# Optimization experiments

Hardware: AMD Instinct MI355X
Metric: run time of the kernel (lower is better)

Reference implementation:

```python
import jax, jax.numpy as jnp
import numpy as np

B, C, H, W = 4, 256, 64, 64
C8 = C // 8

def setup_inputs() -> dict:
    key = jax.random.key(0)
    ks = jax.random.split(key, 7)
    s = 0.05
    return {
        "x": jax.random.normal(ks[0], (B, C, H, W), dtype=jnp.float32),
        "wq": jax.random.normal(ks[1], (C8, C), dtype=jnp.float32) * s,
        "bq": jax.random.normal(ks[2], (C8,), dtype=jnp.float32) * s,
        "wk": jax.random.normal(ks[3], (C8, C), dtype=jnp.float32) * s,
        "bk": jax.random.normal(ks[4], (C8,), dtype=jnp.float32) * s,
        "wv": jax.random.normal(ks[5], (C, C), dtype=jnp.float32) * s,
        "bv": jax.random.normal(ks[6], (C,), dtype=jnp.float32) * s,
    }

def reference(x, wq, bq, wk, bk, wv, bv):
    b, c, h, w = x.shape
    n = h * w
    xf = x.reshape(b, c, n)                                   # [B,C,N]
    q = jnp.einsum('oc,bcn->bon', wq, xf) + bq[:, None]       # [B,C/8,N]
    k = jnp.einsum('oc,bcn->bon', wk, xf) + bk[:, None]       # [B,C/8,N]
    v = jnp.einsum('oc,bcn->bon', wv, xf) + bv[:, None]       # [B,C,N]
    # attention[b, i, j] = softmax_j( q[b,:,i] . k[b,:,j] )  (no scaling, per original)
    scores = jnp.einsum('bon,bom->bnm', q, k)                 # [B,N,N]
    attn = jax.nn.softmax(scores, axis=-1)
    # out[b,c,i] = sum_j v[b,c,j] * attn[b,i,j]
    out = jnp.einsum('bcm,bnm->bcn', v, attn)                 # [B,C,N]
    return out.reshape(b, c, h, w) + x
```

## Files before the change

### kernel.cpp

```cpp
#include <hip/hip_runtime.h>
#include <cstdint>
#include <cstddef>

#define BB 4
#define CC 256
#define NN 4096
#define CO 32

typedef __attribute__((ext_vector_type(8))) short bf8;
typedef __attribute__((ext_vector_type(4))) float f4;
typedef __attribute__((ext_vector_type(16))) float f16f;
typedef __attribute__((ext_vector_type(2))) unsigned int u32x2;

#define AS1 __attribute__((address_space(1)))
#define AS3 __attribute__((address_space(3)))

__device__ __forceinline__ unsigned short f2bf(float f) {
    union { float f; unsigned int u; } c; c.f = f;
    unsigned int r = c.u + 0x7FFFu + ((c.u >> 16) & 1u);
    return (unsigned short)(r >> 16);
}
__device__ __forceinline__ float bf2f(unsigned short b) {
    union { unsigned int u; float f; } c; c.u = ((unsigned int)b) << 16;
    return c.f;
}
__device__ __forceinline__ unsigned int cvt_pk_bf16(float a, float b) {
    unsigned int r;
    asm("v_cvt_pk_bf16_f32 %0, %1, %2" : "=v"(r) : "v"(a), "v"(b));
    return r;
}

__global__ __launch_bounds__(512, 2) void k_prep(
        const float* __restrict__ x,
        const float* __restrict__ wq, const float* __restrict__ bq,
        const float* __restrict__ wk, const float* __restrict__ bk,
        const float* __restrict__ wv, const float* __restrict__ bv,
        unsigned short* __restrict__ q_hi, unsigned short* __restrict__ q_lo,
        unsigned short* __restrict__ k_hi, unsigned short* __restrict__ k_lo,
        unsigned short* __restrict__ vws) {
    __shared__ float xT[64 * 256];
    int blk = blockIdx.x;
    int it = blk & 63, b = blk >> 6;
    int i0 = it * 64;
    int tid = threadIdx.x, w = tid >> 6, lane = tid & 63;
    int lr = lane & 15, lg = lane >> 4;

    {
        const float* xp = x + (size_t)b * CC * NN + i0;
        int cl = tid >> 4;
        int il = (tid & 15) * 4;
#pragma unroll
        for (int pass = 0; pass < 8; ++pass) {
            int c = pass * 32 + cl;
            f4 v = *(const f4*)(xp + (size_t)c * NN + il);
#pragma unroll
            for (int jj = 0; jj < 4; ++jj) {
                int i = il + jj;
                xT[i * 256 + (((c >> 2) ^ (i & 7)) << 2) + (c & 3)] = v[jj];
            }
        }
    }
    __syncthreads();

    if (w < 4) {
        f4 acc[4] = {};
        for (int ks = 0; ks < 8; ++ks) {
            int i = w * 16 + lr;
            int kc = ks * 32 + lg * 8;
            f4 xa = *(const f4*)&xT[i * 256 + (((kc >> 2) ^ (i & 7)) << 2)];
            f4 xb = *(const f4*)&xT[i * 256 + ((((kc >> 2) + 1) ^ (i & 7)) << 2)];
            bf8 ahi, alo;
#pragma unroll
            for (int e = 0; e < 8; ++e) {
                float f = (e < 4) ? xa[e] : xb[e - 4];
                unsigned short hh = f2bf(f);
                ahi[e] = (short)hh;
                alo[e] = (short)f2bf(f - bf2f(hh));
            }
#pragma unroll
            for (int u = 0; u < 4; ++u) {
                int o = u * 16 + lr;
                const float* wrow = (u < 2) ? (wq + (size_t)o * CC)
                                            : (wk + (size_t)(o - 32) * CC);
                bf8 bhi, blo;
#pragma unroll
                for (int e = 0; e < 8; ++e) {
                    float wvv = wrow[ks * 32 + lg * 8 + e];
                    unsigned short hh = f2bf(wvv);
                    bhi[e] = (short)hh;
                    blo[e] = (short)f2bf(wvv - bf2f(hh));
                }
                acc[u] = __builtin_amdgcn_mfma_f32_16x16x32_bf16(alo, bhi, acc[u], 0, 0, 0);
                acc[u] = __builtin_amdgcn_mfma_f32_16x16x32_bf16(ahi, blo, acc[u], 0, 0, 0);
                acc[u] = __builtin_amdgcn_mfma_f32_16x16x32_bf16(ahi, bhi, acc[u], 0, 0, 0);
            }
        }
#pragma unroll
        for (int u = 0; u < 4; ++u) {
            int o = u * 16 + lr;
            float bias = (u < 2) ? bq[o] : bk[o - 32];
#pragma unroll
            for (int r = 0; r < 4; ++r) {
                int i = i0 + w * 16 + lg * 4 + r;
                float v = acc[u][r] + bias;
                unsigned short hh = f2bf(v);
                unsigned short ll = f2bf(v - bf2f(hh));
                if (u < 2) {
                    size_t off = ((size_t)b * NN + i) * CO + o;
                    q_hi[off] = hh; q_lo[off] = ll;
                } else {
                    size_t off = ((size_t)b * NN + i) * CO + (o - 32);
                    k_hi[off] = hh; k_lo[off] = ll;
                }
            }
        }
    } else {
        int cb = (w - 4) * 64;
        f4 acc[4][4];
#pragma unroll
        for (int u = 0; u < 4; ++u) {
            f4 bias4;
#pragma unroll
            for (int r = 0; r < 4; ++r) bias4[r] = bv[cb + u * 16 + lg * 4 + r];
#pragma unroll
            for (int t = 0; t < 4; ++t) acc[u][t] = bias4;
        }
        for (int ks = 0; ks < 8; ++ks) {
            bf8 bfr[4];
#pragma unroll
            for (int t = 0; t < 4; ++t) {
                int i = t * 16 + lr;
                int kc = ks * 32 + lg * 8;
                f4 xa = *(const f4*)&xT[i * 256 + (((kc >> 2) ^ (i & 7)) << 2)];
                f4 xb = *(const f4*)&xT[i * 256 + ((((kc >> 2) + 1) ^ (i & 7)) << 2)];
#pragma unroll
                for (int e = 0; e < 8; ++e)
                    bfr[t][e] = (short)f2bf((e < 4) ? xa[e] : xb[e - 4]);
            }
#pragma unroll
            for (int u = 0; u < 4; ++u) {
                const float* wrow = wv + (size_t)(cb + u * 16 + lr) * CC + ks * 32 + lg * 8;
                bf8 afr;
#pragma unroll
                for (int e = 0; e < 8; ++e) afr[e] = (short)f2bf(wrow[e]);
#pragma unroll
                for (int t = 0; t < 4; ++t)
                    acc[u][t] = __builtin_amdgcn_mfma_f32_16x16x32_bf16(afr, bfr[t], acc[u][t], 0, 0, 0);
            }
        }
#pragma unroll
        for (int u = 0; u < 4; ++u)
#pragma unroll
            for (int t = 0; t < 4; ++t)
#pragma unroll
                for (int r = 0; r < 4; ++r) {
                    int c = cb + u * 16 + lg * 4 + r;
                    vws[((size_t)b * CC + c) * NN + i0 + t * 16 + lr] = f2bf(acc[u][t][r]);
                }
    }
}

__global__ __launch_bounds__(512, 4) void k_attn(
        const unsigned short* __restrict__ q_hi, const unsigned short* __restrict__ q_lo,
        const unsigned short* __restrict__ k_hi, const unsigned short* __restrict__ k_lo,
        const unsigned short* __restrict__ vws,
        const float* __restrict__ x, float* __restrict__ out) {
    __shared__ __align__(16) unsigned short Vt[2][16384];
    __shared__ __align__(16) unsigned short K2[4096];
    __shared__ __align__(16) unsigned short Pt[2048];
    __shared__ float lsum_s[4][32];

    int m = blockIdx.x;
    int xcd = m & 7;
    int b = xcd >> 1;
    int qblk = ((m >> 3) << 1) + (xcd & 1);
    int i0 = qblk * 32;
    int tid = threadIdx.x, w = tid >> 6, lane = tid & 63;
    int lr = lane & 15, lg = lane >> 4, lr7 = lr & 7;
    int qh = w & 1, jq = w >> 1;
    int l31 = lane & 31, hh = lane >> 5;

    bf8 qfh, qfl;
    {
        size_t off = ((size_t)b * NN + i0 + qh * 16 + lr) * CO + lg * 8;
        qfh = *(const bf8*)(q_hi + off);
        qfl = *(const bf8*)(q_lo + off);
    }

    int l3 = lane >> 3, sl = lane & 7;
    int us = sl ^ l3;
    const unsigned short* kbase = (us < 4) ? (k_hi + (size_t)b * NN * CO + us * 8)
                                           : (k_lo + (size_t)b * NN * CO + (us - 4) * 8);
    const unsigned short* ksrc = kbase + (size_t)(w * 8 + l3) * CO;
    const unsigned short* vsrc = vws + ((size_t)b * CC + w * 32 + l3) * NN + us * 8;

    auto stageK = [&](int jt) {
        int j0 = ((jt < 64) ? jt : 63) * 64;
        __builtin_amdgcn_global_load_lds((const AS1 void*)(ksrc + (size_t)j0 * CO),
            (AS3 void*)(&K2[(w * 8) * 64]), 16, 0, 0);
    };
    auto stageV = [&](int jt, int p) {
        int j0 = ((jt < 64) ? jt : 63) * 64;
#pragma unroll
        for (int n = 0; n < 4; ++n) {
            __builtin_amdgcn_global_load_lds((const AS1 void*)(vsrc + (size_t)(n * 8) * NN + j0),
                (AS3 void*)(&Vt[p][(w * 32 + n * 8) * 64]), 16, 0, 0);
        }
    };

    f16f acc = {};
    float lsum = 0.f;

    stageK(0);
    stageV(0, 0);
    __syncthreads();

    int prow_swz = (l31 ^ (l31 >> 3)) & 7;
    int vrow_swz = l31 & 7;

    for (int jt = 0; jt < 64; ++jt) {
        int pv = jt & 1;
        {
            int jl = jq * 16 + lr;
            const unsigned short* Kp = &K2[jl * 64];
            bf8 kfh = *(const bf8*)(Kp + ((lg ^ lr7)) * 8);
            bf8 kfl = *(const bf8*)(Kp + (((4 | lg) ^ lr7)) * 8);
            f4 s = {};
            s = __builtin_amdgcn_mfma_f32_16x16x32_bf16(kfh, qfl, s, 0, 0, 0);
            s = __builtin_amdgcn_mfma_f32_16x16x32_bf16(kfl, qfh, s, 0, 0, 0);
            s = __builtin_amdgcn_mfma_f32_16x16x32_bf16(kfh, qfh, s, 0, 0, 0);
            float e0 = __expf(s[0]), e1 = __expf(s[1]), e2 = __expf(s[2]), e3 = __expf(s[3]);
            lsum += (e0 + e1) + (e2 + e3);
            u32x2 d;
            d[0] = cvt_pk_bf16(e0, e1);
            d[1] = cvt_pk_bf16(e2, e3);
            int row = qh * 16 + lr;
            int swz = (row ^ (row >> 3)) & 7;
            int slot = (jq * 2 + (lg >> 1)) ^ swz;
            *(u32x2*)&Pt[row * 64 + slot * 8 + (lg & 1) * 4] = d;
        }
        __builtin_amdgcn_sched_barrier(0);
        asm volatile("s_waitcnt vmcnt(0) lgkmcnt(0)" ::: "memory");
        __builtin_amdgcn_s_barrier();
        __builtin_amdgcn_sched_barrier(0);
        stageK(jt + 1);
        __builtin_amdgcn_s_setprio(1);
        {
            const unsigned short* Pr = &Pt[l31 * 64];
            const unsigned short* Vr = &Vt[pv][(w * 32 + l31) * 64];
#pragma unroll
            for (int kc = 0; kc < 4; ++kc) {
                bf8 pb = *(const bf8*)(Pr + (((kc * 2 + hh) ^ prow_swz)) * 8);
                bf8 vf = *(const bf8*)(Vr + (((kc * 2 + hh) ^ vrow_swz)) * 8);
                acc = __builtin_amdgcn_mfma_f32_32x32x16_bf16(vf, pb, acc, 0, 0, 0);
            }
        }
        __builtin_amdgcn_s_setprio(0);
        stageV(jt + 1, pv ^ 1);
        __builtin_amdgcn_sched_barrier(0);
        asm volatile("s_waitcnt vmcnt(4) lgkmcnt(0)" ::: "memory");
        __builtin_amdgcn_s_barrier();
        __builtin_amdgcn_sched_barrier(0);
    }

    lsum += __shfl_xor(lsum, 16, 64);
    lsum += __shfl_xor(lsum, 32, 64);
    if (lane < 16) lsum_s[jq][qh * 16 + lane] = lsum;
    __syncthreads();

    float linv = 1.0f / (((lsum_s[0][l31] + lsum_s[1][l31]) +
                          (lsum_s[2][l31] + lsum_s[3][l31])));
    int iq = i0 + l31;
#pragma unroll
    for (int r = 0; r < 16; ++r) {
        int c = w * 32 + (r & 3) + 8 * (r >> 2) + 4 * hh;
        size_t off = ((size_t)(b * CC + c)) * NN + iq;
        out[off] = acc[r] * linv + x[off];
    }
}

extern "C" void kernel_launch(void* const* d_in, const int* in_sizes, int n_in,
                              void* d_out, int out_size, void* d_ws, size_t ws_size,
                              hipStream_t stream) {
    const float* x  = (const float*)d_in[0];
    const float* wq = (const float*)d_in[1];
    const float* bq = (const float*)d_in[2];
    const float* wk = (const float*)d_in[3];
    const float* bk = (const float*)d_in[4];
    const float* wv = (const float*)d_in[5];
    const float* bv = (const float*)d_in[6];
    float* out = (float*)d_out;
    char* ws = (char*)d_ws;
    unsigned short* qh = (unsigned short*)(ws);
    unsigned short* ql = (unsigned short*)(ws + 1048576);
    unsigned short* kh = (unsigned short*)(ws + 2097152);
    unsigned short* kl = (unsigned short*)(ws + 3145728);
    unsigned short* vv = (unsigned short*)(ws + 4194304);

    hipLaunchKernelGGL(k_prep, dim3(256), dim3(512), 0, stream,
                       x, wq, bq, wk, bk, wv, bv, qh, ql, kh, kl, vv);
    hipLaunchKernelGGL(k_attn, dim3(512), dim3(512), 0, stream,
                       qh, ql, kh, kl, vv, x, out);
}
```

Before: 103.5 us.

## Double query tile per block and software-pipeline QK softmax ahead of PV

After: 110.1 us. +6.4%, slower.

```diff
diff --git a/kernel.cpp b/kernel.cpp
--- a/kernel.cpp
+++ b/kernel.cpp
@@ -160,29 +160,30 @@
     }
 }
 
-__global__ __launch_bounds__(512, 4) void k_attn(
+__global__ __launch_bounds__(512, 1) void k_attn(
         const unsigned short* __restrict__ q_hi, const unsigned short* __restrict__ q_lo,
         const unsigned short* __restrict__ k_hi, const unsigned short* __restrict__ k_lo,
         const unsigned short* __restrict__ vws,
         const float* __restrict__ x, float* __restrict__ out) {
     __shared__ __align__(16) unsigned short Vt[2][16384];
-    __shared__ __align__(16) unsigned short K2[4096];
-    __shared__ __align__(16) unsigned short Pt[2048];
-    __shared__ float lsum_s[4][32];
+    __shared__ __align__(16) unsigned short K2[2][4096];
+    __shared__ __align__(16) unsigned short Pt[2][4096];
+    __shared__ float lsum_s[2][64];
 
     int m = blockIdx.x;
     int xcd = m & 7;
     int b = xcd >> 1;
     int qblk = ((m >> 3) << 1) + (xcd & 1);
-    int i0 = qblk * 32;
+    int i0 = qblk * 64;
     int tid = threadIdx.x, w = tid >> 6, lane = tid & 63;
     int lr = lane & 15, lg = lane >> 4, lr7 = lr & 7;
-    int qh = w & 1, jq = w >> 1;
+    int a = w & 3, h = w >> 2;
     int l31 = lane & 31, hh = lane >> 5;
+    int cw = w & 3, qg = w >> 2;
 
     bf8 qfh, qfl;
     {
-        size_t off = ((size_t)b * NN + i0 + qh * 16 + lr) * CO + lg * 8;
+        size_t off = ((size_t)b * NN + i0 + a * 16 + lr) * CO + lg * 8;
         qfh = *(const bf8*)(q_hi + off);
         qfl = *(const bf8*)(q_lo + off);
     }
@@ -194,10 +195,10 @@
     const unsigned short* ksrc = kbase + (size_t)(w * 8 + l3) * CO;
     const unsigned short* vsrc = vws + ((size_t)b * CC + w * 32 + l3) * NN + us * 8;
 
-    auto stageK = [&](int jt) {
+    auto stageK = [&](int jt, int p) {
         int j0 = ((jt < 64) ? jt : 63) * 64;
         __builtin_amdgcn_global_load_lds((const AS1 void*)(ksrc + (size_t)j0 * CO),
-            (AS3 void*)(&K2[(w * 8) * 64]), 16, 0, 0);
+            (AS3 void*)(&K2[p][(w * 8) * 64]), 16, 0, 0);
     };
     auto stageV = [&](int jt, int p) {
         int j0 = ((jt < 64) ? jt : 63) * 64;
@@ -208,21 +209,15 @@
         }
     };
 
-    f16f acc = {};
+    f16f acc0 = {}, acc1 = {};
     float lsum = 0.f;
 
-    stageK(0);
-    stageV(0, 0);
-    __syncthreads();
-
-    int prow_swz = (l31 ^ (l31 >> 3)) & 7;
-    int vrow_swz = l31 & 7;
-
-    for (int jt = 0; jt < 64; ++jt) {
-        int pv = jt & 1;
-        {
-            int jl = jq * 16 + lr;
-            const unsigned short* Kp = &K2[jl * 64];
+    auto S_phase = [&](int js) {
+        int pk = js & 1;
+#pragma unroll
+        for (int t = 0; t < 2; ++t) {
+            int jl = h * 32 + t * 16 + lr;
+            const unsigned short* Kp = &K2[pk][jl * 64];
             bf8 kfh = *(const bf8*)(Kp + ((lg ^ lr7)) * 8);
             bf8 kfl = *(const bf8*)(Kp + (((4 | lg) ^ lr7)) * 8);
             f4 s = {};
@@ -234,48 +229,67 @@
             u32x2 d;
             d[0] = cvt_pk_bf16(e0, e1);
             d[1] = cvt_pk_bf16(e2, e3);
-            int row = qh * 16 + lr;
+            int row = a * 16 + lr;
             int swz = (row ^ (row >> 3)) & 7;
-            int slot = (jq * 2 + (lg >> 1)) ^ swz;
-            *(u32x2*)&Pt[row * 64 + slot * 8 + (lg & 1) * 4] = d;
-        }
+            int slot = (h * 4 + t * 2 + (lg >> 1)) ^ swz;
+            *(u32x2*)&Pt[pk][row * 64 + slot * 8 + (lg & 1) * 4] = d;
+        }
+    };
+    auto PV_phase = [&](int jt) {
+        int pv = jt & 1;
+        int prow = qg * 32 + l31;
+        int pswz = (prow ^ (prow >> 3)) & 7;
+        const unsigned short* Pr  = &Pt[pv][prow * 64];
+        const unsigned short* Vr0 = &Vt[pv][(cw * 64 + l31) * 64];
+        const unsigned short* Vr1 = &Vt[pv][(cw * 64 + 32 + l31) * 64];
+        int vswz = l31 & 7;
+#pragma unroll
+        for (int kc = 0; kc < 4; ++kc) {
+            bf8 pb = *(const bf8*)(Pr  + (((kc * 2 + hh) ^ pswz)) * 8);
+            bf8 v0 = *(const bf8*)(Vr0 + (((kc * 2 + hh) ^ vswz)) * 8);
+            bf8 v1 = *(const bf8*)(Vr1 + (((kc * 2 + hh) ^ vswz)) * 8);
+            acc0 = __builtin_amdgcn_mfma_f32_32x32x16_bf16(v0, pb, acc0, 0, 0, 0);
+            acc1 = __builtin_amdgcn_mfma_f32_32x32x16_bf16(v1, pb, acc1, 0, 0, 0);
+        }
+    };
+
+    stageK(0, 0);
+    stageV(0, 0);
+    __builtin_amdgcn_sched_barrier(0);
+    asm volatile("s_waitcnt vmcnt(0) lgkmcnt(0)" ::: "memory");
+    __builtin_amdgcn_s_barrier();
+    __builtin_amdgcn_sched_barrier(0);
+    stageK(1, 1);
+    S_phase(0);
+
+    for (int jt = 0; jt < 64; ++jt) {
         __builtin_amdgcn_sched_barrier(0);
         asm volatile("s_waitcnt vmcnt(0) lgkmcnt(0)" ::: "memory");
         __builtin_amdgcn_s_barrier();
         __builtin_amdgcn_sched_barrier(0);
-        stageK(jt + 1);
+        stageV(jt + 1, (jt + 1) & 1);
+        stageK(jt + 2, jt & 1);
+        if (jt < 63) S_phase(jt + 1);
         __builtin_amdgcn_s_setprio(1);
-        {
-            const unsigned short* Pr = &Pt[l31 * 64];
-            const unsigned short* Vr = &Vt[pv][(w * 32 + l31) * 64];
-#pragma unroll
-            for (int kc = 0; kc < 4; ++kc) {
-                bf8 pb = *(const bf8*)(Pr + (((kc * 2 + hh) ^ prow_swz)) * 8);
-                bf8 vf = *(const bf8*)(Vr + (((kc * 2 + hh) ^ vrow_swz)) * 8);
-                acc = __builtin_amdgcn_mfma_f32_32x32x16_bf16(vf, pb, acc, 0, 0, 0);
-            }
-        }
+        PV_phase(jt);
         __builtin_amdgcn_s_setprio(0);
-        stageV(jt + 1, pv ^ 1);
-        __builtin_amdgcn_sched_barrier(0);
-        asm volatile("s_waitcnt vmcnt(4) lgkmcnt(0)" ::: "memory");
-        __builtin_amdgcn_s_barrier();
-        __builtin_amdgcn_sched_barrier(0);
     }
 
     lsum += __shfl_xor(lsum, 16, 64);
     lsum += __shfl_xor(lsum, 32, 64);
-    if (lane < 16) lsum_s[jq][qh * 16 + lane] = lsum;
+    if (lane < 16) lsum_s[h][a * 16 + lane] = lsum;
     __syncthreads();
 
-    float linv = 1.0f / (((lsum_s[0][l31] + lsum_s[1][l31]) +
-                          (lsum_s[2][l31] + lsum_s[3][l31])));
-    int iq = i0 + l31;
+    int qloc = qg * 32 + l31;
+    float linv = 1.0f / (lsum_s[0][qloc] + lsum_s[1][qloc]);
+    int iq = i0 + qloc;
 #pragma unroll
     for (int r = 0; r < 16; ++r) {
-        int c = w * 32 + (r & 3) + 8 * (r >> 2) + 4 * hh;
-        size_t off = ((size_t)(b * CC + c)) * NN + iq;
-        out[off] = acc[r] * linv + x[off];
+        int c0 = cw * 64 + (r & 3) + 8 * (r >> 2) + 4 * hh;
+        size_t off0 = ((size_t)(b * CC + c0)) * NN + iq;
+        out[off0] = acc0[r] * linv + x[off0];
+        size_t off1 = ((size_t)(b * CC + c0 + 32)) * NN + iq;
+        out[off1] = acc1[r] * linv + x[off1];
     }
 }
 
@@ -299,6 +313,6 @@
 
     hipLaunchKernelGGL(k_prep, dim3(256), dim3(512), 0, stream,
                        x, wq, bq, wk, bk, wv, bv, qh, ql, kh, kl, vv);
-    hipLaunchKernelGGL(k_attn, dim3(512), dim3(512), 0, stream,
+    hipLaunchKernelGGL(k_attn, dim3(256), dim3(512), 0, stream,
                        qh, ql, kh, kl, vv, x, out);
 }
```

## Retile attention block to 64 queries by 128 channels with register-resident P

Applied to the files above, without the earlier changes.

After: 126.7 us. 22.4% more time.

```diff
diff --git a/kernel.cpp b/kernel.cpp
--- a/kernel.cpp
+++ b/kernel.cpp
@@ -165,26 +165,29 @@
         const unsigned short* __restrict__ k_hi, const unsigned short* __restrict__ k_lo,
         const unsigned short* __restrict__ vws,
         const float* __restrict__ x, float* __restrict__ out) {
-    __shared__ __align__(16) unsigned short Vt[2][16384];
-    __shared__ __align__(16) unsigned short K2[4096];
-    __shared__ __align__(16) unsigned short Pt[2048];
-    __shared__ float lsum_s[4][32];
+    __shared__ __align__(16) unsigned short Vt[2][8192];
+    __shared__ __align__(16) unsigned short K2[2][4096];
+    __shared__ float lsum_s[2][2][32];
 
     int m = blockIdx.x;
     int xcd = m & 7;
     int b = xcd >> 1;
-    int qblk = ((m >> 3) << 1) + (xcd & 1);
-    int i0 = qblk * 32;
+    int t128 = ((m >> 3) << 1) + (xcd & 1);
+    int qblk = t128 >> 1;
+    int hc = t128 & 1;
+    int i0 = qblk * 64;
+    int cb0 = hc * 128;
     int tid = threadIdx.x, w = tid >> 6, lane = tid & 63;
-    int lr = lane & 15, lg = lane >> 4, lr7 = lr & 7;
-    int qh = w & 1, jq = w >> 1;
     int l31 = lane & 31, hh = lane >> 5;
-
-    bf8 qfh, qfl;
+    int qs = w >> 2, js = (w >> 1) & 1, cs = w & 1;
+
+    bf8 qfh0, qfl0, qfh1, qfl1;
     {
-        size_t off = ((size_t)b * NN + i0 + qh * 16 + lr) * CO + lg * 8;
-        qfh = *(const bf8*)(q_hi + off);
-        qfl = *(const bf8*)(q_lo + off);
+        size_t qoff = ((size_t)b * NN + i0 + qs * 32 + l31) * CO + hh * 8;
+        qfh0 = *(const bf8*)(q_hi + qoff);
+        qfl0 = *(const bf8*)(q_lo + qoff);
+        qfh1 = *(const bf8*)(q_hi + qoff + 16);
+        qfl1 = *(const bf8*)(q_lo + qoff + 16);
     }
 
     int l3 = lane >> 3, sl = lane & 7;
@@ -192,90 +195,128 @@
     const unsigned short* kbase = (us < 4) ? (k_hi + (size_t)b * NN * CO + us * 8)
                                            : (k_lo + (size_t)b * NN * CO + (us - 4) * 8);
     const unsigned short* ksrc = kbase + (size_t)(w * 8 + l3) * CO;
-    const unsigned short* vsrc = vws + ((size_t)b * CC + w * 32 + l3) * NN + us * 8;
-
-    auto stageK = [&](int jt) {
+    const unsigned short* vsrc = vws + ((size_t)b * CC + cb0 + w * 16 + l3) * NN + us * 8;
+
+    auto stageK = [&](int jt, int p) {
         int j0 = ((jt < 64) ? jt : 63) * 64;
         __builtin_amdgcn_global_load_lds((const AS1 void*)(ksrc + (size_t)j0 * CO),
-            (AS3 void*)(&K2[(w * 8) * 64]), 16, 0, 0);
+            (AS3 void*)(&K2[p][(w * 8) * 64]), 16, 0, 0);
     };
     auto stageV = [&](int jt, int p) {
         int j0 = ((jt < 64) ? jt : 63) * 64;
 #pragma unroll
-        for (int n = 0; n < 4; ++n) {
+        for (int n = 0; n < 2; ++n) {
             __builtin_amdgcn_global_load_lds((const AS1 void*)(vsrc + (size_t)(n * 8) * NN + j0),
-                (AS3 void*)(&Vt[p][(w * 32 + n * 8) * 64]), 16, 0, 0);
+                (AS3 void*)(&Vt[p][(w * 16 + n * 8) * 64]), 16, 0, 0);
         }
     };
 
-    f16f acc = {};
+    int krow = js * 32 + l31, ksw = krow & 7, koff = krow * 64;
+    int vrow0 = cs * 64 + l31,      vsw0 = vrow0 & 7, voff0 = vrow0 * 64;
+    int vrow1 = cs * 64 + 32 + l31, vsw1 = vrow1 & 7, voff1 = vrow1 * 64;
+
+    f16f acc0 = {}, acc1 = {};
     float lsum = 0.f;
 
-    stageK(0);
+    stageK(0, 0);
     stageV(0, 0);
-    __syncthreads();
-
-    int prow_swz = (l31 ^ (l31 >> 3)) & 7;
-    int vrow_swz = l31 & 7;
+    __builtin_amdgcn_sched_barrier(0);
+    asm volatile("s_waitcnt vmcnt(0) lgkmcnt(0)" ::: "memory");
+    __builtin_amdgcn_s_barrier();
+    __builtin_amdgcn_sched_barrier(0);
 
     for (int jt = 0; jt < 64; ++jt) {
-        int pv = jt & 1;
+        int p = jt & 1;
+        stageK(jt + 1, p ^ 1);
+        stageV(jt + 1, p ^ 1);
+        const unsigned short* Kp = &K2[p][koff];
+        f16f s = {};
         {
-            int jl = jq * 16 + lr;
-            const unsigned short* Kp = &K2[jl * 64];
-            bf8 kfh = *(const bf8*)(Kp + ((lg ^ lr7)) * 8);
-            bf8 kfl = *(const bf8*)(Kp + (((4 | lg) ^ lr7)) * 8);
-            f4 s = {};
-            s = __builtin_amdgcn_mfma_f32_16x16x32_bf16(kfh, qfl, s, 0, 0, 0);
-            s = __builtin_amdgcn_mfma_f32_16x16x32_bf16(kfl, qfh, s, 0, 0, 0);
-            s = __builtin_amdgcn_mfma_f32_16x16x32_bf16(kfh, qfh, s, 0, 0, 0);
-            float e0 = __expf(s[0]), e1 = __expf(s[1]), e2 = __expf(s[2]), e3 = __expf(s[3]);
-            lsum += (e0 + e1) + (e2 + e3);
-            u32x2 d;
-            d[0] = cvt_pk_bf16(e0, e1);
-            d[1] = cvt_pk_bf16(e2, e3);
-            int row = qh * 16 + lr;
-            int swz = (row ^ (row >> 3)) & 7;
-            int slot = (jq * 2 + (lg >> 1)) ^ swz;
-            *(u32x2*)&Pt[row * 64 + slot * 8 + (lg & 1) * 4] = d;
-        }
+            bf8 kfh = *(const bf8*)(Kp + ((0 + hh) ^ ksw) * 8);
+            bf8 kfl = *(const bf8*)(Kp + ((4 + hh) ^ ksw) * 8);
+            s = __builtin_amdgcn_mfma_f32_32x32x16_bf16(kfh, qfl0, s, 0, 0, 0);
+            s = __builtin_amdgcn_mfma_f32_32x32x16_bf16(kfl, qfh0, s, 0, 0, 0);
+            s = __builtin_amdgcn_mfma_f32_32x32x16_bf16(kfh, qfh0, s, 0, 0, 0);
+        }
+        {
+            bf8 kfh = *(const bf8*)(Kp + ((2 + hh) ^ ksw) * 8);
+            bf8 kfl = *(const bf8*)(Kp + ((6 + hh) ^ ksw) * 8);
+            s = __builtin_amdgcn_mfma_f32_32x32x16_bf16(kfh, qfl1, s, 0, 0, 0);
+            s = __builtin_amdgcn_mfma_f32_32x32x16_bf16(kfl, qfh1, s, 0, 0, 0);
+            s = __builtin_amdgcn_mfma_f32_32x32x16_bf16(kfh, qfh1, s, 0, 0, 0);
+        }
+        float e0 = __expf(s[0]),  e1 = __expf(s[1]),  e2 = __expf(s[2]),  e3 = __expf(s[3]);
+        float e4 = __expf(s[4]),  e5 = __expf(s[5]),  e6 = __expf(s[6]),  e7 = __expf(s[7]);
+        float e8 = __expf(s[8]),  e9 = __expf(s[9]),  e10 = __expf(s[10]), e11 = __expf(s[11]);
+        float e12 = __expf(s[12]), e13 = __expf(s[13]), e14 = __expf(s[14]), e15 = __expf(s[15]);
+        lsum += ((e0 + e1) + (e2 + e3)) + ((e4 + e5) + (e6 + e7))
+              + ((e8 + e9) + (e10 + e11)) + ((e12 + e13) + (e14 + e15));
+        __builtin_amdgcn_s_setprio(1);
+        {
+            unsigned int plo0 = cvt_pk_bf16(e0, e1), plo1 = cvt_pk_bf16(e2, e3);
+            unsigned int phi0 = cvt_pk_bf16(e4, e5), phi1 = cvt_pk_bf16(e6, e7);
+            unsigned int s0 = hh ? plo0 : phi0;
+            unsigned int s1 = hh ? plo1 : phi1;
+            unsigned int r0 = __shfl_xor(s0, 32, 64);
+            unsigned int r1 = __shfl_xor(s1, 32, 64);
+            union { unsigned int u[4]; bf8 v; } pb;
+            pb.u[0] = hh ? r0 : plo0;
+            pb.u[1] = hh ? r1 : plo1;
+            pb.u[2] = hh ? phi0 : r0;
+            pb.u[3] = hh ? phi1 : r1;
+            bf8 vf0 = *(const bf8*)&Vt[p][voff0 + (((js * 4 + 0 + hh) ^ vsw0)) * 8];
+            bf8 vf1 = *(const bf8*)&Vt[p][voff1 + (((js * 4 + 0 + hh) ^ vsw1)) * 8];
+            acc0 = __builtin_amdgcn_mfma_f32_32x32x16_bf16(vf0, pb.v, acc0, 0, 0, 0);
+            acc1 = __builtin_amdgcn_mfma_f32_32x32x16_bf16(vf1, pb.v, acc1, 0, 0, 0);
+        }
+        {
+            unsigned int plo0 = cvt_pk_bf16(e8, e9),   plo1 = cvt_pk_bf16(e10, e11);
+            unsigned int phi0 = cvt_pk_bf16(e12, e13), phi1 = cvt_pk_bf16(e14, e15);
+            unsigned int s0 = hh ? plo0 : phi0;
+            unsigned int s1 = hh ? plo1 : phi1;
+            unsigned int r0 = __shfl_xor(s0, 32, 64);
+            unsigned int r1 = __shfl_xor(s1, 32, 64);
+            union { unsigned int u[4]; bf8 v; } pb;
+            pb.u[0] = hh ? r0 : plo0;
+            pb.u[1] = hh ? r1 : plo1;
+            pb.u[2] = hh ? phi0 : r0;
+            pb.u[3] = hh ? phi1 : r1;
+            bf8 vf0 = *(const bf8*)&Vt[p][voff0 + (((js * 4 + 2 + hh) ^ vsw0)) * 8];
+            bf8 vf1 = *(const bf8*)&Vt[p][voff1 + (((js * 4 + 2 + hh) ^ vsw1)) * 8];
+            acc0 = __builtin_amdgcn_mfma_f32_32x32x16_bf16(vf0, pb.v, acc0, 0, 0, 0);
+            acc1 = __builtin_amdgcn_mfma_f32_32x32x16_bf16(vf1, pb.v, acc1, 0, 0, 0);
+        }
+        __builtin_amdgcn_s_setprio(0);
         __builtin_amdgcn_sched_barrier(0);
         asm volatile("s_waitcnt vmcnt(0) lgkmcnt(0)" ::: "memory");
         __builtin_amdgcn_s_barrier();
         __builtin_amdgcn_sched_barrier(0);
-        stageK(jt + 1);
-        __builtin_amdgcn_s_setprio(1);
-        {
-            const unsigned short* Pr = &Pt[l31 * 64];
-            const unsigned short* Vr = &Vt[pv][(w * 32 + l31) * 64];
-#pragma unroll
-            for (int kc = 0; kc < 4; ++kc) {
-                bf8 pb = *(const bf8*)(Pr + (((kc * 2 + hh) ^ prow_swz)) * 8);
-                bf8 vf = *(const bf8*)(Vr + (((kc * 2 + hh) ^ vrow_swz)) * 8);
-                acc = __builtin_amdgcn_mfma_f32_32x32x16_bf16(vf, pb, acc, 0, 0, 0);
-            }
-        }
-        __builtin_amdgcn_s_setprio(0);
-        stageV(jt + 1, pv ^ 1);
-        __builtin_amdgcn_sched_barrier(0);
-        asm volatile("s_waitcnt vmcnt(4) lgkmcnt(0)" ::: "memory");
-        __builtin_amdgcn_s_barrier();
-        __builtin_amdgcn_sched_barrier(0);
-    }
-
-    lsum += __shfl_xor(lsum, 16, 64);
+    }
+
     lsum += __shfl_xor(lsum, 32, 64);
-    if (lane < 16) lsum_s[jq][qh * 16 + lane] = lsum;
+    if (cs == 0 && lane < 32) lsum_s[qs][js][l31] = lsum;
+
+    float* VtF = (float*)&Vt[0][0];
+    int pid = qs * 2 + cs;
+    if (js == 1) {
+#pragma unroll
+        for (int r = 0; r < 16; ++r) {
+            VtF[pid * 2048 + 0    + lane * 16 + r] = acc0[r];
+            VtF[pid * 2048 + 1024 + lane * 16 + r] = acc1[r];
+        }
+    }
     __syncthreads();
-
-    float linv = 1.0f / (((lsum_s[0][l31] + lsum_s[1][l31]) +
-                          (lsum_s[2][l31] + lsum_s[3][l31])));
-    int iq = i0 + l31;
-#pragma unroll
-    for (int r = 0; r < 16; ++r) {
-        int c = w * 32 + (r & 3) + 8 * (r >> 2) + 4 * hh;
-        size_t off = ((size_t)(b * CC + c)) * NN + iq;
-        out[off] = acc[r] * linv + x[off];
+    if (js == 0) {
+        float linv = 1.0f / (lsum_s[qs][0][l31] + lsum_s[qs][1][l31]);
+        int iq = i0 + qs * 32 + l31;
+#pragma unroll
+        for (int r = 0; r < 16; ++r) {
+            int c0 = cb0 + cs * 64 + (r & 3) + 8 * (r >> 2) + 4 * hh;
+            size_t off0 = ((size_t)(b * CC + c0)) * NN + iq;
+            out[off0] = (acc0[r] + VtF[pid * 2048 + lane * 16 + r]) * linv + x[off0];
+            size_t off1 = ((size_t)(b * CC + c0 + 32)) * NN + iq;
+            out[off1] = (acc1[r] + VtF[pid * 2048 + 1024 + lane * 16 + r]) * linv + x[off1];
+        }
     }
 }
 
```
